# Kernel tuning notes

Measured on AMD Instinct MI355X. Metric: run time of the kernel, lower is better.

Reference implementation:

```python
import jax, jax.numpy as jnp
import numpy as np


def setup_inputs() -> dict:
    key = jax.random.key(0)
    inputs = jax.random.normal(key, (8, 2048, 512), dtype=jnp.float32)
    return {"inputs": inputs}


def reference(inputs) -> jnp.ndarray:
    # score[b,i,j] = <x_i, x_j>  (no 1/sqrt(d) scaling in the original)
    score = jnp.einsum("bsd,btd->bst", inputs, inputs)  # [B,S,S]
    distribution = jax.nn.softmax(score, axis=-1)
    # output = distribution @ inputs
    return jnp.einsum("bst,btd->bsd", distribution, inputs)
```

## Files before the change

### kernel.cpp

```cpp
#include <hip/hip_runtime.h>
#include <hip/hip_bf16.h>

#define BATCH 8
#define SEQ   2048
#define DIM   512
#define QB    32
#define KB    64
#define NT    512
#define NKV   (SEQ / KB)

typedef __attribute__((ext_vector_type(8))) short short8;
typedef __attribute__((ext_vector_type(4))) float f32x4;
typedef __attribute__((ext_vector_type(4))) unsigned short ushort4v;

__device__ __forceinline__ unsigned short f2bf(float f) {
    union { float f; unsigned u; } v; v.f = f;
    return (unsigned short)((v.u + 0x7FFFu + ((v.u >> 16) & 1u)) >> 16);
}

__device__ __forceinline__ int swz(int kv) {
    return (8 * (kv & 7)) ^ (16 * ((kv >> 3) & 3)) ^ (64 * ((kv >> 3) & 1));
}

__global__ __launch_bounds__(256)
void prep_kernel(const float* __restrict__ X,
                 unsigned short* __restrict__ Xbf,
                 unsigned short* __restrict__ Xt) {
    __shared__ unsigned short T[64][72];
    const int b  = blockIdx.z;
    const int s0 = blockIdx.x * 64;
    const int d0 = blockIdx.y * 64;
    const int tid = threadIdx.x;
    const float* Xb = X + ((size_t)b * SEQ + s0) * DIM + d0;
    unsigned short* Yb = Xbf + ((size_t)b * SEQ + s0) * DIM + d0;
    #pragma unroll
    for (int r = 0; r < 4; ++r) {
        const int s = (tid >> 4) + r * 16;
        const int d = (tid & 15) * 4;
        float4 v = *(const float4*)(Xb + (size_t)s * DIM + d);
        ushort4v h;
        h[0] = f2bf(v.x); h[1] = f2bf(v.y); h[2] = f2bf(v.z); h[3] = f2bf(v.w);
        *(ushort4v*)(Yb + (size_t)s * DIM + d) = h;
        *(ushort4v*)&T[s][d] = h;
    }
    __syncthreads();
    {
        const int d = tid >> 2;
        const int sc = (tid & 3) * 16;
        unsigned short buf[16];
        #pragma unroll
        for (int j = 0; j < 16; ++j) buf[j] = T[sc + j][d];
        unsigned short* o = Xt + ((size_t)b * DIM + d0 + d) * SEQ + s0 + sc;
        *(short8*)(o)     = *(short8*)&buf[0];
        *(short8*)(o + 8) = *(short8*)&buf[8];
    }
}

__device__ __forceinline__ void stage_K(const unsigned short* __restrict__ Xb,
                                        unsigned short* klds, int t, int w, int lane) {
    const unsigned short* kp = Xb + (size_t)(t * KB) * DIM;
    #pragma unroll
    for (int k = 0; k < 8; ++k) {
        const int kv = k * 8 + w;
        const int dsrc = (lane * 8) ^ swz(kv);
        const unsigned short* g = kp + (size_t)kv * DIM + dsrc;
        unsigned short* l = klds + kv * DIM;
        __builtin_amdgcn_global_load_lds(
            (__attribute__((address_space(1))) void*)(g),
            (__attribute__((address_space(3))) void*)(l), 16, 0, 0);
    }
}

__device__ __forceinline__ void stage_V(const unsigned short* __restrict__ Xtb,
                                        unsigned short* vtlds, int t, int w, int lane) {
    #pragma unroll
    for (int k = 0; k < 8; ++k) {
        const int r = w * 64 + k * 8 + (lane >> 3);
        const int kvsrc = ((lane & 7) * 8) ^ (8 * (r & 7));
        const unsigned short* g = Xtb + (size_t)r * SEQ + t * KB + kvsrc;
        unsigned short* l = vtlds + (w * 64 + k * 8) * KB;
        __builtin_amdgcn_global_load_lds(
            (__attribute__((address_space(1))) void*)(g),
            (__attribute__((address_space(3))) void*)(l), 16, 0, 0);
    }
}

__global__ __launch_bounds__(NT, 2)
void attn_fwd(const unsigned short* __restrict__ Xbf,
              const unsigned short* __restrict__ Xt,
              float* __restrict__ O) {
    const int b   = blockIdx.x & 7;
    const int qt  = blockIdx.x >> 3;
    const int tid = threadIdx.x;
    const int lane = tid & 63;
    const int w    = tid >> 6;
    const int col  = lane & 15;
    const int kgrp = lane >> 4;

    __shared__ alignas(16) unsigned short Klds[KB * DIM];
    __shared__ alignas(16) unsigned short Vtlds[DIM * KB];
    __shared__ alignas(16) float Sbuf[QB][KB + 4];
    __shared__ alignas(16) unsigned short Pfrag[2][2][64][8];
    __shared__ float m_s[QB], l_s[QB], fac_s[QB];

    const unsigned short* Xb  = Xbf + (size_t)b * SEQ * DIM;
    const unsigned short* Xtb = Xt  + (size_t)b * DIM * SEQ;

    const int qs = w >> 2;
    const int kc = w & 3;
    short8 qfrag[16];
    {
        const int qrow = qt * QB + qs * 16 + col;
        const unsigned short* qp = Xb + (size_t)qrow * DIM;
        #pragma unroll
        for (int ks = 0; ks < 16; ++ks)
            qfrag[ks] = *(const short8*)(qp + ks * 32 + kgrp * 8);
    }

    if (tid < QB) { m_s[tid] = -INFINITY; l_s[tid] = 0.f; }

    f32x4 oacc[2][4];
    #pragma unroll
    for (int i = 0; i < 2; ++i)
        #pragma unroll
        for (int j = 0; j < 4; ++j)
            oacc[i][j] = (f32x4){0.f, 0.f, 0.f, 0.f};

    stage_K(Xb,  Klds,  0, w, lane);
    stage_V(Xtb, Vtlds, 0, w, lane);
    asm volatile("s_waitcnt vmcnt(0)" ::: "memory");
    __syncthreads();

    for (int t = 0; t < NKV; ++t) {
        {
            const int kvrow = kc * 16 + col;
            const unsigned short* kbase = &Klds[kvrow * DIM];
            const int sw = swz(kvrow);
            f32x4 sacc = (f32x4){0.f,0.f,0.f,0.f};
            #pragma unroll
            for (int ks = 0; ks < 16; ++ks) {
                short8 kfr = *(const short8*)(kbase + ((ks * 32 + kgrp * 8) ^ sw));
                sacc = __builtin_amdgcn_mfma_f32_16x16x32_bf16(qfrag[ks], kfr, sacc, 0, 0, 0);
            }
            #pragma unroll
            for (int r = 0; r < 4; ++r)
                Sbuf[qs * 16 + kgrp * 4 + r][kc * 16 + col] = sacc[r];
        }
        __syncthreads();

        if (t + 1 < NKV) stage_K(Xb, Klds, t + 1, w, lane);

        {
            const int r = tid >> 4;
            const int c = tid & 15;
            float4 sa = *(const float4*)&Sbuf[r][c * 4];
            float mloc = fmaxf(fmaxf(sa.x, sa.y), fmaxf(sa.z, sa.w));
            mloc = fmaxf(mloc, __shfl_xor(mloc, 1));
            mloc = fmaxf(mloc, __shfl_xor(mloc, 2));
            mloc = fmaxf(mloc, __shfl_xor(mloc, 4));
            mloc = fmaxf(mloc, __shfl_xor(mloc, 8));
            const float mold = m_s[r];
            const float mnew = fmaxf(mold, mloc);
            const float fac  = __expf(mold - mnew);
            float p0 = __expf(sa.x - mnew), p1 = __expf(sa.y - mnew);
            float p2 = __expf(sa.z - mnew), p3 = __expf(sa.w - mnew);
            float lsum = (p0 + p1) + (p2 + p3);
            lsum += __shfl_xor(lsum, 1);
            lsum += __shfl_xor(lsum, 2);
            lsum += __shfl_xor(lsum, 4);
            lsum += __shfl_xor(lsum, 8);
            ushort4v p4;
            p4[0] = f2bf(p0); p4[1] = f2bf(p1); p4[2] = f2bf(p2); p4[3] = f2bf(p3);
            *(ushort4v*)&Pfrag[r >> 4][c >> 3][(r & 15) + 16 * ((c >> 1) & 3)][(c & 1) * 4] = p4;
            if (c == 0) {
                m_s[r] = mnew;
                fac_s[r] = fac;
                l_s[r] = l_s[r] * fac + lsum;
            }
        }
        if (t + 1 < NKV) { asm volatile("s_waitcnt vmcnt(8)" ::: "memory"); }
        else             { asm volatile("s_waitcnt vmcnt(0)" ::: "memory"); }
        __syncthreads();

        #pragma unroll
        for (int q2 = 0; q2 < 2; ++q2) {
            #pragma unroll
            for (int r = 0; r < 4; ++r) {
                const float f = fac_s[q2 * 16 + kgrp * 4 + r];
                #pragma unroll
                for (int dt = 0; dt < 4; ++dt) oacc[q2][dt][r] *= f;
            }
        }
        #pragma unroll
        for (int kc2 = 0; kc2 < 2; ++kc2) {
            const int kvb = kc2 * 32 + kgrp * 8;
            short8 afr[2];
            #pragma unroll
            for (int q2 = 0; q2 < 2; ++q2)
                afr[q2] = *(const short8*)&Pfrag[q2][kc2][lane][0];
            #pragma unroll
            for (int dt = 0; dt < 4; ++dt) {
                const int d = w * 64 + dt * 16 + col;
                const short8 bfr = *(const short8*)&Vtlds[d * KB + (kvb ^ (8 * (d & 7)))];
                #pragma unroll
                for (int q2 = 0; q2 < 2; ++q2)
                    oacc[q2][dt] = __builtin_amdgcn_mfma_f32_16x16x32_bf16(afr[q2], bfr, oacc[q2][dt], 0, 0, 0);
            }
        }
        __syncthreads();

        if (t + 1 < NKV) {
            stage_V(Xtb, Vtlds, t + 1, w, lane);
            asm volatile("s_waitcnt vmcnt(8)" ::: "memory");
            __syncthreads();
        }
    }

    #pragma unroll
    for (int q2 = 0; q2 < 2; ++q2) {
        #pragma unroll
        for (int r = 0; r < 4; ++r) {
            const int row = q2 * 16 + kgrp * 4 + r;
            const float inv = 1.f / l_s[row];
            float* op = O + ((size_t)b * SEQ + qt * QB + row) * DIM + w * 64 + col;
            #pragma unroll
            for (int dt = 0; dt < 4; ++dt)
                op[dt * 16] = oacc[q2][dt][r] * inv;
        }
    }
}

extern "C" void kernel_launch(void* const* d_in, const int* in_sizes, int n_in,
                              void* d_out, int out_size, void* d_ws, size_t ws_size,
                              hipStream_t stream) {
    const float* X = (const float*)d_in[0];
    float* Out = (float*)d_out;
    unsigned short* Xbf = (unsigned short*)d_ws;
    unsigned short* Xt  = Xbf + (size_t)BATCH * SEQ * DIM;

    dim3 pgrid(SEQ / 64, DIM / 64, BATCH);
    hipLaunchKernelGGL(prep_kernel, pgrid, dim3(256), 0, stream, X, Xbf, Xt);

    dim3 grid(BATCH * (SEQ / QB));
    dim3 block(NT);
    hipLaunchKernelGGL(attn_fwd, grid, block, 0, stream, Xbf, Xt, Out);
}
```

Baseline: 196.0 us.

## Double query tile to 64 rows so each warp reuses K/V fragments

Raises the query block from 32 to 64 rows. Each warp now computes two 16-row query subtiles against the same K fragment, and the PV product runs over four query subtiles per V fragment. This halves the number of blocks and the K/V global and LDS traffic per output row. Softmax is reorganised to 8 threads per row with 8 elements each, writing full short8 P fragments. In exchange it roughly doubles register use for the Q fragments and accumulators under unchanged launch bounds, which risks spills. It also leaves only one wave of blocks across the CUs.

```diff
diff --git a/kernel.cpp b/kernel.cpp
--- a/kernel.cpp
+++ b/kernel.cpp
@@ -4,7 +4,7 @@
 #define BATCH 8
 #define SEQ   2048
 #define DIM   512
-#define QB    32
+#define QB    64
 #define KB    64
 #define NT    512
 #define NKV   (SEQ / KB)
@@ -100,28 +100,29 @@
     __shared__ alignas(16) unsigned short Klds[KB * DIM];
     __shared__ alignas(16) unsigned short Vtlds[DIM * KB];
     __shared__ alignas(16) float Sbuf[QB][KB + 4];
-    __shared__ alignas(16) unsigned short Pfrag[2][2][64][8];
+    __shared__ alignas(16) unsigned short Pfrag[4][2][64][8];
     __shared__ float m_s[QB], l_s[QB], fac_s[QB];
 
     const unsigned short* Xb  = Xbf + (size_t)b * SEQ * DIM;
     const unsigned short* Xtb = Xt  + (size_t)b * DIM * SEQ;
 
-    const int qs = w >> 2;
+    const int qh = w >> 2;
     const int kc = w & 3;
-    short8 qfrag[16];
-    {
-        const int qrow = qt * QB + qs * 16 + col;
+    short8 qfrag[2][16];
+    #pragma unroll
+    for (int qq = 0; qq < 2; ++qq) {
+        const int qrow = qt * QB + qh * 32 + qq * 16 + col;
         const unsigned short* qp = Xb + (size_t)qrow * DIM;
         #pragma unroll
         for (int ks = 0; ks < 16; ++ks)
-            qfrag[ks] = *(const short8*)(qp + ks * 32 + kgrp * 8);
+            qfrag[qq][ks] = *(const short8*)(qp + ks * 32 + kgrp * 8);
     }
 
     if (tid < QB) { m_s[tid] = -INFINITY; l_s[tid] = 0.f; }
 
-    f32x4 oacc[2][4];
-    #pragma unroll
-    for (int i = 0; i < 2; ++i)
+    f32x4 oacc[4][4];
+    #pragma unroll
+    for (int i = 0; i < 4; ++i)
         #pragma unroll
         for (int j = 0; j < 4; ++j)
             oacc[i][j] = (f32x4){0.f, 0.f, 0.f, 0.f};
@@ -136,42 +137,49 @@
             const int kvrow = kc * 16 + col;
             const unsigned short* kbase = &Klds[kvrow * DIM];
             const int sw = swz(kvrow);
-            f32x4 sacc = (f32x4){0.f,0.f,0.f,0.f};
+            f32x4 sacc0 = (f32x4){0.f,0.f,0.f,0.f};
+            f32x4 sacc1 = (f32x4){0.f,0.f,0.f,0.f};
             #pragma unroll
             for (int ks = 0; ks < 16; ++ks) {
                 short8 kfr = *(const short8*)(kbase + ((ks * 32 + kgrp * 8) ^ sw));
-                sacc = __builtin_amdgcn_mfma_f32_16x16x32_bf16(qfrag[ks], kfr, sacc, 0, 0, 0);
-            }
-            #pragma unroll
-            for (int r = 0; r < 4; ++r)
-                Sbuf[qs * 16 + kgrp * 4 + r][kc * 16 + col] = sacc[r];
+                sacc0 = __builtin_amdgcn_mfma_f32_16x16x32_bf16(qfrag[0][ks], kfr, sacc0, 0, 0, 0);
+                sacc1 = __builtin_amdgcn_mfma_f32_16x16x32_bf16(qfrag[1][ks], kfr, sacc1, 0, 0, 0);
+            }
+            #pragma unroll
+            for (int r = 0; r < 4; ++r) {
+                Sbuf[qh * 32 + 0  + kgrp * 4 + r][kc * 16 + col] = sacc0[r];
+                Sbuf[qh * 32 + 16 + kgrp * 4 + r][kc * 16 + col] = sacc1[r];
+            }
         }
         __syncthreads();
 
         if (t + 1 < NKV) stage_K(Xb, Klds, t + 1, w, lane);
 
         {
-            const int r = tid >> 4;
-            const int c = tid & 15;
-            float4 sa = *(const float4*)&Sbuf[r][c * 4];
-            float mloc = fmaxf(fmaxf(sa.x, sa.y), fmaxf(sa.z, sa.w));
+            const int r = tid >> 3;
+            const int c = tid & 7;
+            float4 sa = *(const float4*)&Sbuf[r][c * 8];
+            float4 sb = *(const float4*)&Sbuf[r][c * 8 + 4];
+            float mloc = fmaxf(fmaxf(fmaxf(sa.x, sa.y), fmaxf(sa.z, sa.w)),
+                               fmaxf(fmaxf(sb.x, sb.y), fmaxf(sb.z, sb.w)));
             mloc = fmaxf(mloc, __shfl_xor(mloc, 1));
             mloc = fmaxf(mloc, __shfl_xor(mloc, 2));
             mloc = fmaxf(mloc, __shfl_xor(mloc, 4));
-            mloc = fmaxf(mloc, __shfl_xor(mloc, 8));
             const float mold = m_s[r];
             const float mnew = fmaxf(mold, mloc);
             const float fac  = __expf(mold - mnew);
             float p0 = __expf(sa.x - mnew), p1 = __expf(sa.y - mnew);
             float p2 = __expf(sa.z - mnew), p3 = __expf(sa.w - mnew);
-            float lsum = (p0 + p1) + (p2 + p3);
+            float p4 = __expf(sb.x - mnew), p5 = __expf(sb.y - mnew);
+            float p6 = __expf(sb.z - mnew), p7 = __expf(sb.w - mnew);
+            float lsum = ((p0 + p1) + (p2 + p3)) + ((p4 + p5) + (p6 + p7));
             lsum += __shfl_xor(lsum, 1);
             lsum += __shfl_xor(lsum, 2);
             lsum += __shfl_xor(lsum, 4);
-            lsum += __shfl_xor(lsum, 8);
-            ushort4v p4;
-            p4[0] = f2bf(p0); p4[1] = f2bf(p1); p4[2] = f2bf(p2); p4[3] = f2bf(p3);
-            *(ushort4v*)&Pfrag[r >> 4][c >> 3][(r & 15) + 16 * ((c >> 1) & 3)][(c & 1) * 4] = p4;
+            short8 p8;
+            p8[0] = f2bf(p0); p8[1] = f2bf(p1); p8[2] = f2bf(p2); p8[3] = f2bf(p3);
+            p8[4] = f2bf(p4); p8[5] = f2bf(p5); p8[6] = f2bf(p6); p8[7] = f2bf(p7);
+            *(short8*)&Pfrag[r >> 4][c >> 2][(r & 15) + 16 * (c & 3)][0] = p8;
             if (c == 0) {
                 m_s[r] = mnew;
                 fac_s[r] = fac;
@@ -183,7 +191,7 @@
         __syncthreads();
 
         #pragma unroll
-        for (int q2 = 0; q2 < 2; ++q2) {
+        for (int q2 = 0; q2 < 4; ++q2) {
             #pragma unroll
             for (int r = 0; r < 4; ++r) {
                 const float f = fac_s[q2 * 16 + kgrp * 4 + r];
@@ -194,16 +202,16 @@
         #pragma unroll
         for (int kc2 = 0; kc2 < 2; ++kc2) {
             const int kvb = kc2 * 32 + kgrp * 8;
-            short8 afr[2];
-            #pragma unroll
-            for (int q2 = 0; q2 < 2; ++q2)
+            short8 afr[4];
+            #pragma unroll
+            for (int q2 = 0; q2 < 4; ++q2)
                 afr[q2] = *(const short8*)&Pfrag[q2][kc2][lane][0];
             #pragma unroll
             for (int dt = 0; dt < 4; ++dt) {
                 const int d = w * 64 + dt * 16 + col;
                 const short8 bfr = *(const short8*)&Vtlds[d * KB + (kvb ^ (8 * (d & 7)))];
                 #pragma unroll
-                for (int q2 = 0; q2 < 2; ++q2)
+                for (int q2 = 0; q2 < 4; ++q2)
                     oacc[q2][dt] = __builtin_amdgcn_mfma_f32_16x16x32_bf16(afr[q2], bfr, oacc[q2][dt], 0, 0, 0);
             }
         }
@@ -217,7 +225,7 @@
     }
 
     #pragma unroll
-    for (int q2 = 0; q2 < 2; ++q2) {
+    for (int q2 = 0; q2 < 4; ++q2) {
         #pragma unroll
         for (int r = 0; r < 4; ++r) {
             const int row = q2 * 16 + kgrp * 4 + r;
```

Result: slower. 265.2 us (+35.3%).

## Keep online softmax in registers via transposed MFMA, drop score buffer

Applied to the files above, without the earlier changes.

The QK^T MFMA operands are swapped so each lane holds scores for one query row across four keys. This lets the row max and sum be computed with cross-lane shuffles plus a small per-wave partial-max exchange, replacing the full score LDS buffer and the separate softmax pass. The running max and sum live in registers, and the PV product is reorganised so each wave owns 16 query rows by 128 output columns, which also allows float4 output stores. In exchange, each wave holds more accumulator registers, and the per-wave partial sums must be combined at the end.

```diff
diff --git a/kernel.cpp b/kernel.cpp
--- a/kernel.cpp
+++ b/kernel.cpp
@@ -96,18 +96,18 @@
     const int w    = tid >> 6;
     const int col  = lane & 15;
     const int kgrp = lane >> 4;
+    const int qs = w >> 2;
+    const int kx = w & 3;
 
     __shared__ alignas(16) unsigned short Klds[KB * DIM];
     __shared__ alignas(16) unsigned short Vtlds[DIM * KB];
-    __shared__ alignas(16) float Sbuf[QB][KB + 4];
-    __shared__ alignas(16) unsigned short Pfrag[2][2][64][8];
-    __shared__ float m_s[QB], l_s[QB], fac_s[QB];
+    __shared__ alignas(16) unsigned short Pfrag[2][16][64];
+    __shared__ alignas(16) float mpart[2][16][4];
+    __shared__ alignas(16) float lpart[2][16][4];
 
     const unsigned short* Xb  = Xbf + (size_t)b * SEQ * DIM;
     const unsigned short* Xtb = Xt  + (size_t)b * DIM * SEQ;
 
-    const int qs = w >> 2;
-    const int kc = w & 3;
     short8 qfrag[16];
     {
         const int qrow = qt * QB + qs * 16 + col;
@@ -117,14 +117,12 @@
             qfrag[ks] = *(const short8*)(qp + ks * 32 + kgrp * 8);
     }
 
-    if (tid < QB) { m_s[tid] = -INFINITY; l_s[tid] = 0.f; }
-
-    f32x4 oacc[2][4];
-    #pragma unroll
-    for (int i = 0; i < 2; ++i)
-        #pragma unroll
-        for (int j = 0; j < 4; ++j)
-            oacc[i][j] = (f32x4){0.f, 0.f, 0.f, 0.f};
+    float m_reg = -INFINITY;
+    float l_reg = 0.f;
+
+    f32x4 oacc[8];
+    #pragma unroll
+    for (int i = 0; i < 8; ++i) oacc[i] = (f32x4){0.f, 0.f, 0.f, 0.f};
 
     stage_K(Xb,  Klds,  0, w, lane);
     stage_V(Xtb, Vtlds, 0, w, lane);
@@ -132,50 +130,46 @@
     __syncthreads();
 
     for (int t = 0; t < NKV; ++t) {
+        f32x4 sacc = (f32x4){0.f, 0.f, 0.f, 0.f};
         {
-            const int kvrow = kc * 16 + col;
+            const int kvrow = kx * 16 + col;
             const unsigned short* kbase = &Klds[kvrow * DIM];
             const int sw = swz(kvrow);
-            f32x4 sacc = (f32x4){0.f,0.f,0.f,0.f};
             #pragma unroll
             for (int ks = 0; ks < 16; ++ks) {
                 short8 kfr = *(const short8*)(kbase + ((ks * 32 + kgrp * 8) ^ sw));
-                sacc = __builtin_amdgcn_mfma_f32_16x16x32_bf16(qfrag[ks], kfr, sacc, 0, 0, 0);
+                sacc = __builtin_amdgcn_mfma_f32_16x16x32_bf16(kfr, qfrag[ks], sacc, 0, 0, 0);
             }
+        }
+        {
+            float pm = fmaxf(fmaxf(sacc[0], sacc[1]), fmaxf(sacc[2], sacc[3]));
+            pm = fmaxf(pm, __shfl_xor(pm, 16));
+            pm = fmaxf(pm, __shfl_xor(pm, 32));
+            if (lane < 16) mpart[qs][lane][kx] = pm;
+        }
+        __syncthreads();
+        if (t + 1 < NKV) stage_K(Xb, Klds, t + 1, w, lane);
+
+        {
+            float4 mp = *(const float4*)&mpart[qs][col][0];
+            const float mnew = fmaxf(fmaxf(fmaxf(mp.x, mp.y), fmaxf(mp.z, mp.w)), m_reg);
+            const float fac  = __expf(m_reg - mnew);
+            m_reg = mnew;
+            const float p0 = __expf(sacc[0] - mnew);
+            const float p1 = __expf(sacc[1] - mnew);
+            const float p2 = __expf(sacc[2] - mnew);
+            const float p3 = __expf(sacc[3] - mnew);
+            float ps = (p0 + p1) + (p2 + p3);
+            ps += __shfl_xor(ps, 16);
+            ps += __shfl_xor(ps, 32);
+            l_reg = l_reg * fac + ps;
+            ushort4v pw;
+            pw[0] = f2bf(p0); pw[1] = f2bf(p1); pw[2] = f2bf(p2); pw[3] = f2bf(p3);
+            *(ushort4v*)&Pfrag[qs][col][(kx * 16 + kgrp * 4) ^ (8 * (col & 7))] = pw;
             #pragma unroll
-            for (int r = 0; r < 4; ++r)
-                Sbuf[qs * 16 + kgrp * 4 + r][kc * 16 + col] = sacc[r];
-        }
-        __syncthreads();
-
-        if (t + 1 < NKV) stage_K(Xb, Klds, t + 1, w, lane);
-
-        {
-            const int r = tid >> 4;
-            const int c = tid & 15;
-            float4 sa = *(const float4*)&Sbuf[r][c * 4];
-            float mloc = fmaxf(fmaxf(sa.x, sa.y), fmaxf(sa.z, sa.w));
-            mloc = fmaxf(mloc, __shfl_xor(mloc, 1));
-            mloc = fmaxf(mloc, __shfl_xor(mloc, 2));
-            mloc = fmaxf(mloc, __shfl_xor(mloc, 4));
-            mloc = fmaxf(mloc, __shfl_xor(mloc, 8));
-            const float mold = m_s[r];
-            const float mnew = fmaxf(mold, mloc);
-            const float fac  = __expf(mold - mnew);
-            float p0 = __expf(sa.x - mnew), p1 = __expf(sa.y - mnew);
-            float p2 = __expf(sa.z - mnew), p3 = __expf(sa.w - mnew);
-            float lsum = (p0 + p1) + (p2 + p3);
-            lsum += __shfl_xor(lsum, 1);
-            lsum += __shfl_xor(lsum, 2);
-            lsum += __shfl_xor(lsum, 4);
-            lsum += __shfl_xor(lsum, 8);
-            ushort4v p4;
-            p4[0] = f2bf(p0); p4[1] = f2bf(p1); p4[2] = f2bf(p2); p4[3] = f2bf(p3);
-            *(ushort4v*)&Pfrag[r >> 4][c >> 3][(r & 15) + 16 * ((c >> 1) & 3)][(c & 1) * 4] = p4;
-            if (c == 0) {
-                m_s[r] = mnew;
-                fac_s[r] = fac;
-                l_s[r] = l_s[r] * fac + lsum;
+            for (int dt = 0; dt < 8; ++dt) {
+                oacc[dt][0] *= fac; oacc[dt][1] *= fac;
+                oacc[dt][2] *= fac; oacc[dt][3] *= fac;
             }
         }
         if (t + 1 < NKV) { asm volatile("s_waitcnt vmcnt(8)" ::: "memory"); }
@@ -183,28 +177,15 @@
         __syncthreads();
 
         #pragma unroll
-        for (int q2 = 0; q2 < 2; ++q2) {
+        for (int s = 0; s < 2; ++s) {
+            const short8 pfr = *(const short8*)
+                &Pfrag[qs][col][(s * 32 + kgrp * 8) ^ (8 * (col & 7))];
             #pragma unroll
-            for (int r = 0; r < 4; ++r) {
-                const float f = fac_s[q2 * 16 + kgrp * 4 + r];
-                #pragma unroll
-                for (int dt = 0; dt < 4; ++dt) oacc[q2][dt][r] *= f;
-            }
-        }
-        #pragma unroll
-        for (int kc2 = 0; kc2 < 2; ++kc2) {
-            const int kvb = kc2 * 32 + kgrp * 8;
-            short8 afr[2];
-            #pragma unroll
-            for (int q2 = 0; q2 < 2; ++q2)
-                afr[q2] = *(const short8*)&Pfrag[q2][kc2][lane][0];
-            #pragma unroll
-            for (int dt = 0; dt < 4; ++dt) {
-                const int d = w * 64 + dt * 16 + col;
-                const short8 bfr = *(const short8*)&Vtlds[d * KB + (kvb ^ (8 * (d & 7)))];
-                #pragma unroll
-                for (int q2 = 0; q2 < 2; ++q2)
-                    oacc[q2][dt] = __builtin_amdgcn_mfma_f32_16x16x32_bf16(afr[q2], bfr, oacc[q2][dt], 0, 0, 0);
+            for (int dt = 0; dt < 8; ++dt) {
+                const int d = kx * 128 + dt * 16 + col;
+                const short8 vfr = *(const short8*)
+                    &Vtlds[d * KB + ((s * 32 + kgrp * 8) ^ (8 * (d & 7)))];
+                oacc[dt] = __builtin_amdgcn_mfma_f32_16x16x32_bf16(vfr, pfr, oacc[dt], 0, 0, 0);
             }
         }
         __syncthreads();
@@ -216,16 +197,20 @@
         }
     }
 
-    #pragma unroll
-    for (int q2 = 0; q2 < 2; ++q2) {
-        #pragma unroll
-        for (int r = 0; r < 4; ++r) {
-            const int row = q2 * 16 + kgrp * 4 + r;
-            const float inv = 1.f / l_s[row];
-            float* op = O + ((size_t)b * SEQ + qt * QB + row) * DIM + w * 64 + col;
-            #pragma unroll
-            for (int dt = 0; dt < 4; ++dt)
-                op[dt * 16] = oacc[q2][dt][r] * inv;
+    __syncthreads();
+    if (lane < 16) lpart[qs][lane][kx] = l_reg;
+    __syncthreads();
+    {
+        float4 lp = *(const float4*)&lpart[qs][col][0];
+        const float inv = 1.f / ((lp.x + lp.y) + (lp.z + lp.w));
+        float* op = O + ((size_t)b * SEQ + qt * QB + qs * 16 + col) * DIM
+                      + kx * 128 + kgrp * 4;
+        #pragma unroll
+        for (int dt = 0; dt < 8; ++dt) {
+            float4 o4;
+            o4.x = oacc[dt][0] * inv; o4.y = oacc[dt][1] * inv;
+            o4.z = oacc[dt][2] * inv; o4.w = oacc[dt][3] * inv;
+            *(float4*)(op + dt * 16) = o4;
         }
     }
 }
```

Measured after the change: 184.0 us. 6.2% less time.
